# Optimization experiments

Measured on AMD Instinct MI355X. Metric: run time of the kernel, lower is better.

## Reference

```python
import jax, jax.numpy as jnp
import numpy as np

B, I, O, G = 262144, 3, 64, 128


def setup_inputs() -> dict:
    key = jax.random.key(0)
    kx, kc = jax.random.split(key)
    x = jax.random.uniform(kx, (1, B, I), dtype=jnp.float32)  # coords in [0,1)
    coeffs = jax.random.normal(kc, (2, O, I, G), dtype=jnp.float32) / (
        np.float32(np.sqrt(I) * np.sqrt(G))
    )
    bias = jnp.zeros((1, O), dtype=jnp.float32)
    return {"x": x, "coeffs": coeffs, "bias": bias}


def reference(x, coeffs, bias):
    # x: (1, B, I); coeffs: (2, O, I, G); bias: (1, O)
    b, i = x.shape[1], x.shape[2]
    two, o, _, g = coeffs.shape
    k = jnp.arange(1, g + 1, dtype=x.dtype)          # (G,)
    kx = x.reshape(b, i, 1) * k                      # (B, I, G)
    cosf = jnp.cos(kx).reshape(b, i * g)             # (B, I*G)
    sinf = jnp.sin(kx).reshape(b, i * g)             # (B, I*G)
    w = coeffs.reshape(2, o, i * g)                  # (2, O, I*G)
    # sum over (input_dim, gridsize) fused as one GEMM per trig branch
    out = cosf @ w[0].T + sinf @ w[1].T + bias       # (B, O)
    return out
```

## Files before the change

kernel.cpp:

```cpp
#include <hip/hip_runtime.h>
#include <hip/hip_bf16.h>

typedef __attribute__((ext_vector_type(8))) short short8;
typedef __attribute__((ext_vector_type(4))) float f32x4;
typedef __attribute__((ext_vector_type(2))) float f32x2;

#define NROWS   262144
#define ODIM    64
#define NBLOCKS 256
#define TPB     1024
#define INV2PI  0.15915494309189535f

__device__ __forceinline__ float cos2pi(float f){ float r; asm("v_cos_f32 %0, %1" : "=v"(r) : "v"(f)); return r; }
__device__ __forceinline__ float sin2pi(float f){ float r; asm("v_sin_f32 %0, %1" : "=v"(r) : "v"(f)); return r; }

__device__ __forceinline__ short bf16_of(float f){
    union { __hip_bfloat16 h; short s; } u;
    u.h = __float2bfloat16(f);
    return u.s;
}

extern "C" __global__ void __launch_bounds__(TPB, 4)
__attribute__((amdgpu_waves_per_eu(4, 4)))
fourier_mfma(const float* __restrict__ x,
             const float* __restrict__ coeffs,
             const float* __restrict__ bias,
             float* __restrict__ out)
{
    __shared__ short8 Wlds[24 * 4 * 64];

    const int tid = threadIdx.x;

    for (int fl = tid; fl < 24*4*64; fl += TPB) {
        const int ks = fl >> 8;
        const int nt = (fl >> 6) & 3;
        const int ln = fl & 63;
        const int o  = nt*16 + (ln & 15);
        const int kg = ln >> 4;
        union { short8 v; short s[8]; } fr;
        #pragma unroll
        for (int h = 0; h < 2; ++h) {
            const int kb  = ks*32 + h*16;
            const int br  = (kb >= 384) ? 1 : 0;
            const int rem = kb - br*384;
            const int ii  = rem >> 7;
            const int g0  = (rem & 127) + kg*4;
            const float* wp = coeffs + (((br*ODIM + o)*3 + ii) << 7) + g0;
            #pragma unroll
            for (int j = 0; j < 4; ++j) fr.s[h*4 + j] = bf16_of(wp[j]);
        }
        Wlds[fl] = fr.v;
    }
    __syncthreads();

    const int lane = tid & 63;
    const int wid  = tid >> 6;
    const int mrow = lane & 15;
    const int kgrp = lane >> 4;
    const float hs = (float)(4*kgrp + 1);

    float bcol[4];
    #pragma unroll
    for (int nt = 0; nt < 4; ++nt) bcol[nt] = bias[nt*16 + mrow];

    const int unit = blockIdx.x * 16 + wid;
    const int base = unit * 64;

    #pragma unroll 1
    for (int rg = 0; rg < 2; ++rg) {
        const int rowA = base + (rg*2 + 0)*16 + mrow;
        const int rowB = base + (rg*2 + 1)*16 + mrow;

        f32x2 xr[3];
        #pragma unroll
        for (int i = 0; i < 3; ++i)
            xr[i] = (f32x2){ x[rowA*3 + i] * INV2PI, x[rowB*3 + i] * INV2PI };

        f32x4 acc[2][4];
        #pragma unroll
        for (int rr = 0; rr < 2; ++rr)
            #pragma unroll
            for (int nt = 0; nt < 4; ++nt)
                acc[rr][nt] = (f32x4){0.f, 0.f, 0.f, 0.f};

        f32x2 cvp, svp, c16p, s16p, stc, sts;

        #pragma unroll 1
        for (int kk = 0; kk < 12; ++kk) {
            short8 bfr[8];
            #pragma unroll
            for (int nt = 0; nt < 4; ++nt) {
                bfr[nt]     = Wlds[(kk*4 + nt)*64 + lane];
                bfr[4 + nt] = Wlds[((kk + 12)*4 + nt)*64 + lane];
            }

            if ((kk & 3) == 0) {
                const int i = kk >> 2;
                const f32x2 a = xr[i];
                cvp = (f32x2){ cos2pi(a.x), cos2pi(a.y) };
                svp = (f32x2){ sin2pi(a.x), sin2pi(a.y) };
                f32x2 t = (f32x2){ 16.f*a.x, 16.f*a.y };
                t.x -= floorf(t.x); t.y -= floorf(t.y);
                c16p = (f32x2){ cos2pi(t.x), cos2pi(t.y) };
                s16p = (f32x2){ sin2pi(t.x), sin2pi(t.y) };
                f32x2 u = (f32x2){ hs*a.x, hs*a.y };
                u.x -= floorf(u.x); u.y -= floorf(u.y);
                stc = (f32x2){ cos2pi(u.x), cos2pi(u.y) };
                sts = (f32x2){ sin2pi(u.x), sin2pi(u.y) };
            }

            union { short8 v; short s[8]; } fc[2], fs[2];
            #pragma unroll
            for (int h = 0; h < 2; ++h) {
                f32x2 c = stc, s = sts;
                fc[0].s[h*4] = bf16_of(c.x); fc[1].s[h*4] = bf16_of(c.y);
                fs[0].s[h*4] = bf16_of(s.x); fs[1].s[h*4] = bf16_of(s.y);
                #pragma unroll
                for (int j = 1; j < 4; ++j) {
                    const f32x2 cn = c*cvp - s*svp;
                    const f32x2 sn = s*cvp + c*svp;
                    c = cn; s = sn;
                    fc[0].s[h*4+j] = bf16_of(c.x); fc[1].s[h*4+j] = bf16_of(c.y);
                    fs[0].s[h*4+j] = bf16_of(s.x); fs[1].s[h*4+j] = bf16_of(s.y);
                }
                const f32x2 nc = stc*c16p - sts*s16p;
                const f32x2 ns = sts*c16p + stc*s16p;
                stc = nc; sts = ns;
            }

            #pragma unroll
            for (int nt = 0; nt < 4; ++nt) {
                #pragma unroll
                for (int rr = 0; rr < 2; ++rr) {
                    acc[rr][nt] = __builtin_amdgcn_mfma_f32_16x16x32_bf16(fc[rr].v, bfr[nt],     acc[rr][nt], 0, 0, 0);
                    acc[rr][nt] = __builtin_amdgcn_mfma_f32_16x16x32_bf16(fs[rr].v, bfr[4 + nt], acc[rr][nt], 0, 0, 0);
                }
            }
        }

        #pragma unroll
        for (int rr = 0; rr < 2; ++rr) {
            const int row0 = base + (rg*2 + rr)*16 + kgrp*4;
            #pragma unroll
            for (int nt = 0; nt < 4; ++nt) {
                #pragma unroll
                for (int q = 0; q < 4; ++q) {
                    out[(row0 + q)*ODIM + nt*16 + mrow] = acc[rr][nt][q] + bcol[nt];
                }
            }
        }
    }
}

extern "C" void kernel_launch(void* const* d_in, const int* in_sizes, int n_in,
                              void* d_out, int out_size, void* d_ws, size_t ws_size,
                              hipStream_t stream) {
    const float* x      = (const float*)d_in[0];
    const float* coeffs = (const float*)d_in[1];
    const float* bias   = (const float*)d_in[2];
    float* out = (float*)d_out;
    (void)in_sizes; (void)n_in; (void)out_size; (void)d_ws; (void)ws_size;
    hipLaunchKernelGGL(fourier_mfma, dim3(NBLOCKS), dim3(TPB), 0, stream, x, coeffs, bias, out);
}
```

Before: 41.41 us.

## Switch MFMA operands to fp16 and generate trig features with packed half2 recurrences

```diff
diff --git a/kernel.cpp b/kernel.cpp
--- a/kernel.cpp
+++ b/kernel.cpp
@@ -1,9 +1,11 @@
 #include <hip/hip_runtime.h>
-#include <hip/hip_bf16.h>
+#include <hip/hip_fp16.h>
 
 typedef __attribute__((ext_vector_type(8))) short short8;
+typedef __attribute__((ext_vector_type(8))) _Float16 half8;
 typedef __attribute__((ext_vector_type(4))) float f32x4;
 typedef __attribute__((ext_vector_type(2))) float f32x2;
+typedef __attribute__((ext_vector_type(4))) unsigned int u32x4;
 
 #define NROWS   262144
 #define ODIM    64
@@ -14,11 +16,18 @@
 __device__ __forceinline__ float cos2pi(float f){ float r; asm("v_cos_f32 %0, %1" : "=v"(r) : "v"(f)); return r; }
 __device__ __forceinline__ float sin2pi(float f){ float r; asm("v_sin_f32 %0, %1" : "=v"(r) : "v"(f)); return r; }
 
-__device__ __forceinline__ short bf16_of(float f){
-    union { __hip_bfloat16 h; short s; } u;
-    u.h = __float2bfloat16(f);
-    return u.s;
-}
+__device__ __forceinline__ short f16_of(float f){
+    union { _Float16 h; short s; } u; u.h = (_Float16)f; return u.s; }
+__device__ __forceinline__ unsigned h2b(__half2 h){
+    union { __half2 h; unsigned u; } x; x.h = h; return x.u; }
+__device__ __forceinline__ half8 u4h(u32x4 v){ union{u32x4 u; half8 h;} x; x.u = v; return x.h; }
+__device__ __forceinline__ half8 s8h(short8 v){ union{short8 s; half8 h;} x; x.s = v; return x.h; }
+
+#define ADV(C, S, RC, RS, RN) do {                       \
+    const __half2 _cn = __hfma2(C, RC, __hmul2(S, RN));  \
+    const __half2 _sn = __hfma2(S, RC, __hmul2(C, RS));  \
+    C = _cn; S = _sn;                                    \
+} while (0)
 
 extern "C" __global__ void __launch_bounds__(TPB, 4)
 __attribute__((amdgpu_waves_per_eu(4, 4)))
@@ -47,7 +56,7 @@
             const int g0  = (rem & 127) + kg*4;
             const float* wp = coeffs + (((br*ODIM + o)*3 + ii) << 7) + g0;
             #pragma unroll
-            for (int j = 0; j < 4; ++j) fr.s[h*4 + j] = bf16_of(wp[j]);
+            for (int j = 0; j < 4; ++j) fr.s[h*4 + j] = f16_of(wp[j]);
         }
         Wlds[fl] = fr.v;
     }
@@ -83,7 +92,9 @@
             for (int nt = 0; nt < 4; ++nt)
                 acc[rr][nt] = (f32x4){0.f, 0.f, 0.f, 0.f};
 
-        f32x2 cvp, svp, c16p, s16p, stc, sts;
+        __half2 C0, S0, C1, S1;
+        __half2 c2h0, s2h0, n2h0, c14h0, s14h0, n14h0;
+        __half2 c2h1, s2h1, n2h1, c14h1, s14h1, n14h1;
 
         #pragma unroll 1
         for (int kk = 0; kk < 12; ++kk) {
@@ -97,44 +108,59 @@
             if ((kk & 3) == 0) {
                 const int i = kk >> 2;
                 const f32x2 a = xr[i];
-                cvp = (f32x2){ cos2pi(a.x), cos2pi(a.y) };
-                svp = (f32x2){ sin2pi(a.x), sin2pi(a.y) };
-                f32x2 t = (f32x2){ 16.f*a.x, 16.f*a.y };
-                t.x -= floorf(t.x); t.y -= floorf(t.y);
-                c16p = (f32x2){ cos2pi(t.x), cos2pi(t.y) };
-                s16p = (f32x2){ sin2pi(t.x), sin2pi(t.y) };
-                f32x2 u = (f32x2){ hs*a.x, hs*a.y };
-                u.x -= floorf(u.x); u.y -= floorf(u.y);
-                stc = (f32x2){ cos2pi(u.x), cos2pi(u.y) };
-                sts = (f32x2){ sin2pi(u.x), sin2pi(u.y) };
+                {
+                    const float av = a.x;
+                    float u0 = hs*av;        u0 -= floorf(u0);
+                    float u1 = (hs+1.f)*av;  u1 -= floorf(u1);
+                    C0 = __floats2half2_rn(cos2pi(u0), cos2pi(u1));
+                    S0 = __floats2half2_rn(sin2pi(u0), sin2pi(u1));
+                    float t2 = 2.f*av;       t2 -= floorf(t2);
+                    const float c2 = cos2pi(t2), s2 = sin2pi(t2);
+                    float t14 = 14.f*av;     t14 -= floorf(t14);
+                    const float c14 = cos2pi(t14), s14 = sin2pi(t14);
+                    c2h0  = __float2half2_rn(c2);   s2h0  = __float2half2_rn(s2);
+                    n2h0  = __float2half2_rn(-s2);
+                    c14h0 = __float2half2_rn(c14);  s14h0 = __float2half2_rn(s14);
+                    n14h0 = __float2half2_rn(-s14);
+                }
+                {
+                    const float av = a.y;
+                    float u0 = hs*av;        u0 -= floorf(u0);
+                    float u1 = (hs+1.f)*av;  u1 -= floorf(u1);
+                    C1 = __floats2half2_rn(cos2pi(u0), cos2pi(u1));
+                    S1 = __floats2half2_rn(sin2pi(u0), sin2pi(u1));
+                    float t2 = 2.f*av;       t2 -= floorf(t2);
+                    const float c2 = cos2pi(t2), s2 = sin2pi(t2);
+                    float t14 = 14.f*av;     t14 -= floorf(t14);
+                    const float c14 = cos2pi(t14), s14 = sin2pi(t14);
+                    c2h1  = __float2half2_rn(c2);   s2h1  = __float2half2_rn(s2);
+                    n2h1  = __float2half2_rn(-s2);
+                    c14h1 = __float2half2_rn(c14);  s14h1 = __float2half2_rn(s14);
+                    n14h1 = __float2half2_rn(-s14);
+                }
             }
 
-            union { short8 v; short s[8]; } fc[2], fs[2];
-            #pragma unroll
-            for (int h = 0; h < 2; ++h) {
-                f32x2 c = stc, s = sts;
-                fc[0].s[h*4] = bf16_of(c.x); fc[1].s[h*4] = bf16_of(c.y);
-                fs[0].s[h*4] = bf16_of(s.x); fs[1].s[h*4] = bf16_of(s.y);
-                #pragma unroll
-                for (int j = 1; j < 4; ++j) {
-                    const f32x2 cn = c*cvp - s*svp;
-                    const f32x2 sn = s*cvp + c*svp;
-                    c = cn; s = sn;
-                    fc[0].s[h*4+j] = bf16_of(c.x); fc[1].s[h*4+j] = bf16_of(c.y);
-                    fs[0].s[h*4+j] = bf16_of(s.x); fs[1].s[h*4+j] = bf16_of(s.y);
-                }
-                const f32x2 nc = stc*c16p - sts*s16p;
-                const f32x2 ns = sts*c16p + stc*s16p;
-                stc = nc; sts = ns;
-            }
+            u32x4 FCA, FCB, FSA, FSB;
+            FCA.x = h2b(C0); FSA.x = h2b(S0); FCB.x = h2b(C1); FSB.x = h2b(S1);
+            ADV(C0, S0, c2h0,  s2h0,  n2h0);  ADV(C1, S1, c2h1,  s2h1,  n2h1);
+            FCA.y = h2b(C0); FSA.y = h2b(S0); FCB.y = h2b(C1); FSB.y = h2b(S1);
+            ADV(C0, S0, c14h0, s14h0, n14h0); ADV(C1, S1, c14h1, s14h1, n14h1);
+            FCA.z = h2b(C0); FSA.z = h2b(S0); FCB.z = h2b(C1); FSB.z = h2b(S1);
+            ADV(C0, S0, c2h0,  s2h0,  n2h0);  ADV(C1, S1, c2h1,  s2h1,  n2h1);
+            FCA.w = h2b(C0); FSA.w = h2b(S0); FCB.w = h2b(C1); FSB.w = h2b(S1);
+            ADV(C0, S0, c14h0, s14h0, n14h0); ADV(C1, S1, c14h1, s14h1, n14h1);
+
+            const half8 fAc = u4h(FCA);
+            const half8 fBc = u4h(FCB);
+            const half8 fAs = u4h(FSA);
+            const half8 fBs = u4h(FSB);
 
             #pragma unroll
             for (int nt = 0; nt < 4; ++nt) {
-                #pragma unroll
-                for (int rr = 0; rr < 2; ++rr) {
-                    acc[rr][nt] = __builtin_amdgcn_mfma_f32_16x16x32_bf16(fc[rr].v, bfr[nt],     acc[rr][nt], 0, 0, 0);
-                    acc[rr][nt] = __builtin_amdgcn_mfma_f32_16x16x32_bf16(fs[rr].v, bfr[4 + nt], acc[rr][nt], 0, 0, 0);
-                }
+                acc[0][nt] = __builtin_amdgcn_mfma_f32_16x16x32_f16(fAc, s8h(bfr[nt]),   acc[0][nt], 0, 0, 0);
+                acc[1][nt] = __builtin_amdgcn_mfma_f32_16x16x32_f16(fBc, s8h(bfr[nt]),   acc[1][nt], 0, 0, 0);
+                acc[0][nt] = __builtin_amdgcn_mfma_f32_16x16x32_f16(fAs, s8h(bfr[4+nt]), acc[0][nt], 0, 0, 0);
+                acc[1][nt] = __builtin_amdgcn_mfma_f32_16x16x32_f16(fBs, s8h(bfr[4+nt]), acc[1][nt], 0, 0, 0);
             }
         }
 
```

After: 38.72 us, median of 2. 1.07x faster.
